# Kernel optimization log

Measured on AMD Instinct MI355X. Metric: run time of the kernel, lower is better.

Reference implementation:

```python
import jax, jax.numpy as jnp
import numpy as np

N = 50000      # nodes
E = 800000     # edges (avg degree 16)
D = 128        # enc_input_dim
H = 4          # enc_num_heads
C = 32         # enc_hidden_dim (per head)
OUT = 64       # linear_output_dim
NEG_SLOPE = 0.2


def setup_inputs() -> dict:
    key = jax.random.key(0)
    ks = jax.random.split(key, 12)
    def glorot(k, shape, fan):
        return (jax.random.normal(k, shape, jnp.float32) / np.sqrt(fan)).astype(jnp.float32)
    x = jax.random.normal(ks[0], (N, D), jnp.float32)
    edge_index = jax.random.randint(ks[1], (2, E), 0, N, dtype=jnp.int64)
    # GAT layer 0: in=D, out=C per head, heads=H, concat -> H*C
    W0 = glorot(ks[2], (D, H * C), D)
    att_src0 = glorot(ks[3], (H, C), C)
    att_dst0 = glorot(ks[4], (H, C), C)
    b0 = jnp.zeros((H * C,), jnp.float32)
    # GAT layer 1: in=H*C, out=D, heads=1
    W1 = glorot(ks[5], (H * C, D), H * C)
    att_src1 = glorot(ks[6], (1, D), D)
    att_dst1 = glorot(ks[7], (1, D), D)
    b1 = jnp.zeros((D,), jnp.float32)
    # projection heads
    Wn = glorot(ks[8], (D, OUT), D)
    bn = jnp.zeros((OUT,), jnp.float32)
    We = glorot(ks[9], (D, OUT), D)
    be = jnp.zeros((OUT,), jnp.float32)
    return dict(x=x, edge_index=edge_index,
                W0=W0, att_src0=att_src0, att_dst0=att_dst0, b0=b0,
                W1=W1, att_src1=att_src1, att_dst1=att_dst1, b1=b1,
                Wn=Wn, bn=bn, We=We, be=be)


def gat_conv(x, src, dst, W, att_s, att_d, b):
    # PyG GATConv: project, per-head attention logits, LeakyReLU,
    # softmax over incoming edges per destination node, scatter-add aggregate.
    n = x.shape[0]
    heads, ch = att_s.shape
    xl = (x @ W).reshape(n, heads, ch)                       # [N,H,C]
    a_s = jnp.einsum('nhc,hc->nh', xl, att_s)                # [N,H]
    a_d = jnp.einsum('nhc,hc->nh', xl, att_d)                # [N,H]
    alpha = jax.nn.leaky_relu(a_s[src] + a_d[dst], NEG_SLOPE)  # [E',H]
    amax = jax.lax.stop_gradient(jax.ops.segment_max(alpha, dst, num_segments=n))
    ex = jnp.exp(alpha - amax[dst])
    denom = jax.ops.segment_sum(ex, dst, num_segments=n)
    w = ex / (denom[dst] + 1e-16)                            # [E',H]
    out = jax.ops.segment_sum(xl[src] * w[:, :, None], dst, num_segments=n)
    return out.reshape(n, heads * ch) + b


def reference(x, edge_index, W0, att_src0, att_dst0, b0,
              W1, att_src1, att_dst1, b1, Wn, bn, We, be):
    n = x.shape[0]
    loop = jnp.arange(n, dtype=edge_index.dtype)             # PyG add_self_loops
    src = jnp.concatenate([edge_index[0], loop])
    dst = jnp.concatenate([edge_index[1], loop])
    h = jax.nn.relu(gat_conv(x, src, dst, W0, att_src0, att_dst0, b0))
    h = jax.nn.relu(gat_conv(h, src, dst, W1, att_src1, att_dst1, b1))
    h_neighbor = h @ Wn + bn
    h_ego = x @ We + be
    return (h_ego, h_neighbor)
```

## Files before the change

kernel.cpp:

```cpp
#include <hip/hip_runtime.h>


#define LEAKY_SLOPE 0.2f
#define BUCKET_CAP 64

typedef __attribute__((ext_vector_type(8))) short s16x8;
typedef __attribute__((ext_vector_type(4))) float f32x4;

static __device__ __forceinline__ unsigned short f2bf(float f)
{
    unsigned x = __float_as_uint(f);
    unsigned r = (x + 0x7fffu + ((x >> 16) & 1u)) >> 16;
    return (unsigned short)r;
}
static __device__ __forceinline__ float bfhi(unsigned u) { return __uint_as_float(u & 0xffff0000u); }
static __device__ __forceinline__ float bflo(unsigned u) { return __uint_as_float(u << 16); }

__global__ __launch_bounds__(256) void init_k(const float* __restrict__ W0,
                                              const float* __restrict__ W1,
                                              const float* __restrict__ Wn,
                                              const float* __restrict__ We,
                                              unsigned short* __restrict__ P0,
                                              unsigned short* __restrict__ P1,
                                              unsigned short* __restrict__ Pn,
                                              unsigned short* __restrict__ Pe,
                                              int4* __restrict__ curs4, int nz4)
{
    int gid = blockIdx.x * 256 + threadIdx.x;
    if (gid < nz4) {
        curs4[gid] = make_int4(0, 0, 0, 0);
        return;
    }
    int idx = gid - nz4;
    if (idx < 49152) {
        const float* S; unsigned short* D; int BN; int local;
        if (idx < 16384)      { S = W0; D = P0; BN = 128; local = idx; }
        else if (idx < 32768) { S = W1; D = P1; BN = 128; local = idx - 16384; }
        else if (idx < 40960) { S = Wn; D = Pn; BN = 64;  local = idx - 32768; }
        else                  { S = We; D = Pe; BN = 64;  local = idx - 40960; }
        int k = local / BN, nn = local % BN;
        D[(((k >> 3) * BN + nn) * 8) + (k & 7)] = f2bf(S[local]);
    }
}

template<int HATT, bool AF32>
static __device__ __forceinline__ void gemm128_body(int tile,
                                                    const void* __restrict__ Ab,
                                                    const unsigned short* __restrict__ Bp,
                                                    unsigned short* __restrict__ Cb,
                                                    const float* __restrict__ ats,
                                                    const float* __restrict__ atd,
                                                    float* __restrict__ a_s,
                                                    float* __restrict__ a_d, int n,
                                                    char* __restrict__ sm)
{
    constexpr int BN = 128;
    constexpr int APITCH = 144;
    constexpr int BPITCH = BN + 2;

    unsigned short* As = (unsigned short*)sm;
    unsigned short* Bs = (unsigned short*)(sm + 64 * APITCH * 2);
    float* smS = (float*)(sm + 64 * APITCH * 2 + 16 * BPITCH * 8 * 2);
    float* smD = smS + 128;

    const int t  = threadIdx.x;
    const int rb = tile * 64;

#pragma unroll
    for (int i = 0; i < 4; ++i) {
        int q = t + i * 256;
        int r = q >> 4;
        int c = (q & 15) * 8;
        int gr = rb + r;
        if (AF32) {
            uint4 o = make_uint4(0u, 0u, 0u, 0u);
            if (gr < n) {
                const float* src = (const float*)Ab + (size_t)gr * 128 + c;
                float4 v0 = *(const float4*)src;
                float4 v1 = *(const float4*)(src + 4);
                o.x = (unsigned)f2bf(v0.x) | ((unsigned)f2bf(v0.y) << 16);
                o.y = (unsigned)f2bf(v0.z) | ((unsigned)f2bf(v0.w) << 16);
                o.z = (unsigned)f2bf(v1.x) | ((unsigned)f2bf(v1.y) << 16);
                o.w = (unsigned)f2bf(v1.z) | ((unsigned)f2bf(v1.w) << 16);
            }
            *(uint4*)(As + r * APITCH + c) = o;
        } else {
            float4 v = make_float4(0.f, 0.f, 0.f, 0.f);
            if (gr < n) v = *(const float4*)((const unsigned short*)Ab + (size_t)gr * 128 + c);
            *(float4*)(As + r * APITCH + c) = v;
        }
    }
#pragma unroll
    for (int i = 0; i < 8; ++i) {
        int ge = t + i * 256;
        int o = ge / BN, nn = ge % BN;
        *(float4*)(Bs + ((size_t)o * BPITCH + nn) * 8) = *(const float4*)(Bp + (size_t)ge * 8);
    }
    __syncthreads();

    const int w = t >> 6, lane = t & 63;
    const int m = lane & 15, quad = lane >> 4;
    const int wc = w & 1, wr = w >> 1;
    const int row0 = wr * 32;
    const int col0 = wc * 64;

    f32x4 acc[2][4];
#pragma unroll
    for (int rt = 0; rt < 2; ++rt)
#pragma unroll
        for (int c = 0; c < 4; ++c) acc[rt][c] = (f32x4){0.f, 0.f, 0.f, 0.f};

    s16x8 a[2][4];
#pragma unroll
    for (int rt = 0; rt < 2; ++rt)
#pragma unroll
        for (int kk = 0; kk < 4; ++kk)
            a[rt][kk] = *(const s16x8*)(As + (row0 + rt * 16 + m) * APITCH + kk * 32 + quad * 8);

#pragma unroll
    for (int kk = 0; kk < 4; ++kk)
#pragma unroll
        for (int c = 0; c < 4; ++c) {
            s16x8 b = *(const s16x8*)(Bs + ((size_t)(kk * 4 + quad) * BPITCH + col0 + c * 16 + m) * 8);
#pragma unroll
            for (int rt = 0; rt < 2; ++rt)
                acc[rt][c] = __builtin_amdgcn_mfma_f32_16x16x32_bf16(a[rt][kk], b, acc[rt][c], 0, 0, 0);
        }

#pragma unroll
    for (int rt = 0; rt < 2; ++rt)
#pragma unroll
        for (int c = 0; c < 4; ++c)
#pragma unroll
            for (int r = 0; r < 4; ++r) {
                int row = rb + row0 + rt * 16 + quad * 4 + r;
                int colg = col0 + c * 16 + m;
                if (row < n) Cb[(size_t)row * 128 + colg] = f2bf(acc[rt][c][r]);
            }

    float atsv[4], atdv[4];
#pragma unroll
    for (int c = 0; c < 4; ++c) {
        atsv[c] = ats[col0 + c * 16 + m];
        atdv[c] = atd[col0 + c * 16 + m];
    }
    if (HATT == 4) {
#pragma unroll
        for (int rt = 0; rt < 2; ++rt)
#pragma unroll
            for (int r = 0; r < 4; ++r)
#pragma unroll
                for (int hb = 0; hb < 2; ++hb) {
                    float ps = acc[rt][2*hb][r] * atsv[2*hb] + acc[rt][2*hb+1][r] * atsv[2*hb+1];
                    float pd = acc[rt][2*hb][r] * atdv[2*hb] + acc[rt][2*hb+1][r] * atdv[2*hb+1];
#pragma unroll
                    for (int off = 1; off < 16; off <<= 1) {
                        ps += __shfl_xor(ps, off);
                        pd += __shfl_xor(pd, off);
                    }
                    int row = rb + row0 + rt * 16 + quad * 4 + r;
                    if (m == 0 && row < n) {
                        a_s[(size_t)row * 4 + 2*wc + hb] = ps;
                        a_d[(size_t)row * 4 + 2*wc + hb] = pd;
                    }
                }
    }
    if (HATT == 1) {
#pragma unroll
        for (int rt = 0; rt < 2; ++rt)
#pragma unroll
            for (int r = 0; r < 4; ++r) {
                float ps = 0.f, pd = 0.f;
#pragma unroll
                for (int c = 0; c < 4; ++c) {
                    ps = fmaf(acc[rt][c][r], atsv[c], ps);
                    pd = fmaf(acc[rt][c][r], atdv[c], pd);
                }
#pragma unroll
                for (int off = 1; off < 16; off <<= 1) {
                    ps += __shfl_xor(ps, off);
                    pd += __shfl_xor(pd, off);
                }
                int lrow = row0 + rt * 16 + quad * 4 + r;
                if (m == 0) { smS[lrow * 2 + wc] = ps; smD[lrow * 2 + wc] = pd; }
            }
        __syncthreads();
        if (t < 64) {
            int row = rb + t;
            if (row < n) {
                a_s[row] = smS[t * 2 + 0] + smS[t * 2 + 1];
                a_d[row] = smD[t * 2 + 0] + smD[t * 2 + 1];
            }
        }
    }
}

template<bool AF32>
static __device__ __forceinline__ void proj64_body(int tile,
                                                   const void* __restrict__ Ab,
                                                   const unsigned short* __restrict__ Bp,
                                                   const float* __restrict__ bias,
                                                   float* __restrict__ Cf, int n,
                                                   char* __restrict__ sm)
{
    constexpr int BN = 64;
    constexpr int APITCH = 144;
    constexpr int BPITCH = BN + 2;

    unsigned short* As = (unsigned short*)sm;
    unsigned short* Bs = (unsigned short*)(sm + 64 * APITCH * 2);

    const int t  = threadIdx.x;
    const int rb = tile * 64;

#pragma unroll
    for (int i = 0; i < 4; ++i) {
        int q = t + i * 256;
        int r = q >> 4;
        int c = (q & 15) * 8;
        int gr = rb + r;
        if (AF32) {
            uint4 o = make_uint4(0u, 0u, 0u, 0u);
            if (gr < n) {
                const float* src = (const float*)Ab + (size_t)gr * 128 + c;
                float4 v0 = *(const float4*)src;
                float4 v1 = *(const float4*)(src + 4);
                o.x = (unsigned)f2bf(v0.x) | ((unsigned)f2bf(v0.y) << 16);
                o.y = (unsigned)f2bf(v0.z) | ((unsigned)f2bf(v0.w) << 16);
                o.z = (unsigned)f2bf(v1.x) | ((unsigned)f2bf(v1.y) << 16);
                o.w = (unsigned)f2bf(v1.z) | ((unsigned)f2bf(v1.w) << 16);
            }
            *(uint4*)(As + r * APITCH + c) = o;
        } else {
            float4 v = make_float4(0.f, 0.f, 0.f, 0.f);
            if (gr < n) v = *(const float4*)((const unsigned short*)Ab + (size_t)gr * 128 + c);
            *(float4*)(As + r * APITCH + c) = v;
        }
    }
#pragma unroll
    for (int i = 0; i < 4; ++i) {
        int ge = t + i * 256;
        int o = ge / BN, nn = ge % BN;
        *(float4*)(Bs + ((size_t)o * BPITCH + nn) * 8) = *(const float4*)(Bp + (size_t)ge * 8);
    }
    __syncthreads();

    const int w = t >> 6, lane = t & 63;
    const int m = lane & 15, quad = lane >> 4;
    const int row0 = w * 16;

    f32x4 acc[4];
#pragma unroll
    for (int c = 0; c < 4; ++c) acc[c] = (f32x4){0.f, 0.f, 0.f, 0.f};

    s16x8 a[4];
#pragma unroll
    for (int kk = 0; kk < 4; ++kk)
        a[kk] = *(const s16x8*)(As + (row0 + m) * APITCH + kk * 32 + quad * 8);

#pragma unroll
    for (int kk = 0; kk < 4; ++kk)
#pragma unroll
        for (int c = 0; c < 4; ++c) {
            s16x8 b = *(const s16x8*)(Bs + ((size_t)(kk * 4 + quad) * BPITCH + c * 16 + m) * 8);
            acc[c] = __builtin_amdgcn_mfma_f32_16x16x32_bf16(a[kk], b, acc[c], 0, 0, 0);
        }

#pragma unroll
    for (int c = 0; c < 4; ++c)
#pragma unroll
        for (int r = 0; r < 4; ++r) {
            int row = rb + row0 + quad * 4 + r;
            int colg = c * 16 + m;
            if (row < n) Cf[(size_t)row * BN + colg] = acc[c][r] + bias[colg];
        }
}

__global__ __launch_bounds__(256) void build_k(const float* __restrict__ x,
                                               const unsigned short* __restrict__ P0,
                                               const unsigned short* __restrict__ Pe,
                                               unsigned short* __restrict__ xlb,
                                               const float* __restrict__ ats,
                                               const float* __restrict__ atd,
                                               float* __restrict__ a_s,
                                               float* __restrict__ a_d,
                                               const float* __restrict__ be,
                                               float* __restrict__ Ce,
                                               const int* __restrict__ ei,
                                               int* __restrict__ curs,
                                               unsigned short* __restrict__ col,
                                               int E, int n,
                                               int scatBlocks, int gemmBlocks)
{
    extern __shared__ char sm[];
    int b = blockIdx.x;
    if (b < scatBlocks) {
        int t8 = (b * 256 + threadIdx.x) * 8;
        if (t8 < E) {
            if ((E & 7) == 0) {
                int4 s0 = *(const int4*)(ei + t8);
                int4 s1 = *(const int4*)(ei + t8 + 4);
                int4 d0 = *(const int4*)(ei + E + t8);
                int4 d1 = *(const int4*)(ei + E + t8 + 4);
                int p0 = atomicAdd(&curs[d0.x << 4], 1);
                int p1 = atomicAdd(&curs[d0.y << 4], 1);
                int p2 = atomicAdd(&curs[d0.z << 4], 1);
                int p3 = atomicAdd(&curs[d0.w << 4], 1);
                int p4 = atomicAdd(&curs[d1.x << 4], 1);
                int p5 = atomicAdd(&curs[d1.y << 4], 1);
                int p6 = atomicAdd(&curs[d1.z << 4], 1);
                int p7 = atomicAdd(&curs[d1.w << 4], 1);
                if (p0 < BUCKET_CAP) col[(d0.x << 6) + p0] = (unsigned short)s0.x;
                if (p1 < BUCKET_CAP) col[(d0.y << 6) + p1] = (unsigned short)s0.y;
                if (p2 < BUCKET_CAP) col[(d0.z << 6) + p2] = (unsigned short)s0.z;
                if (p3 < BUCKET_CAP) col[(d0.w << 6) + p3] = (unsigned short)s0.w;
                if (p4 < BUCKET_CAP) col[(d1.x << 6) + p4] = (unsigned short)s1.x;
                if (p5 < BUCKET_CAP) col[(d1.y << 6) + p5] = (unsigned short)s1.y;
                if (p6 < BUCKET_CAP) col[(d1.z << 6) + p6] = (unsigned short)s1.z;
                if (p7 < BUCKET_CAP) col[(d1.w << 6) + p7] = (unsigned short)s1.w;
            } else {
                int lim = (t8 + 8 < E) ? t8 + 8 : E;
                for (int e = t8; e < lim; ++e) {
                    int s = ei[e], d = ei[E + e];
                    int p = atomicAdd(&curs[d << 4], 1);
                    if (p < BUCKET_CAP) col[(d << 6) + p] = (unsigned short)s;
                }
            }
        }
    } else if (b < scatBlocks + gemmBlocks) {
        gemm128_body<4, true>(b - scatBlocks, x, P0, xlb, ats, atd, a_s, a_d, n, sm);
    } else {
        proj64_body<true>(b - scatBlocks - gemmBlocks, x, Pe, be, Ce, n, sm);
    }
}

__global__ __launch_bounds__(256) void gemm1_k(const unsigned short* __restrict__ Ab,
                                               const unsigned short* __restrict__ Bp,
                                               unsigned short* __restrict__ Cb,
                                               const float* __restrict__ ats,
                                               const float* __restrict__ atd,
                                               float* __restrict__ a_s,
                                               float* __restrict__ a_d, int n)
{
    extern __shared__ char sm[];
    gemm128_body<1, false>(blockIdx.x, Ab, Bp, Cb, ats, atd, a_s, a_d, n, sm);
}

__global__ __launch_bounds__(256) void projN_k(const unsigned short* __restrict__ Ab,
                                               const unsigned short* __restrict__ Bp,
                                               const float* __restrict__ bias,
                                               float* __restrict__ Cf, int n)
{
    extern __shared__ char sm[];
    proj64_body<false>(blockIdx.x, Ab, Bp, bias, Cf, n, sm);
}

template<int H>
__global__ __launch_bounds__(256) void agg_k(const unsigned short* __restrict__ xlb,
                                             const float* __restrict__ a_s,
                                             const float* __restrict__ a_d,
                                             const int* __restrict__ curs,
                                             const unsigned short* __restrict__ col,
                                             const float* __restrict__ bias,
                                             unsigned short* __restrict__ outb, int n)
{
    int node = (blockIdx.x * 256 + threadIdx.x) >> 6;
    int lane = threadIdx.x & 63;
    if (node >= n) return;
    const int sub = lane >> 5, sl = lane & 31;
    const int h = (H == 1) ? 0 : (sl >> 3);
    float ad = a_d[(size_t)node * H + h];
    int m = curs[node << 4];
    if (m > BUCKET_CAP) m = BUCKET_CAP;
    float a0 = 0.f, a1 = 0.f, a2 = 0.f, a3 = 0.f, den = 0.f;
    const unsigned short* xlj = xlb + 4 * sl;

    if (m > 0) {
        int p0 = node << 6;
        int cv = col[p0 + (lane < m ? lane : m - 1)];
        int j = 0;
        for (; j + 16 <= m; j += 16) {
            int jb = j + 8 * sub;
            int s[8]; float as[8]; uint2 uv[8];
#pragma unroll
            for (int q = 0; q < 8; ++q) s[q] = __shfl(cv, jb + q);
#pragma unroll
            for (int q = 0; q < 8; ++q) as[q] = a_s[(size_t)s[q] * H + h];
#pragma unroll
            for (int q = 0; q < 8; ++q) uv[q] = *(const uint2*)(xlj + (size_t)s[q] * 128);
#pragma unroll
            for (int q = 0; q < 8; ++q) {
                float al = as[q] + ad;
                al = (al >= 0.f) ? al : LEAKY_SLOPE * al;
                float w = __expf(al);
                a0 = fmaf(w, bflo(uv[q].x), a0);
                a1 = fmaf(w, bfhi(uv[q].x), a1);
                a2 = fmaf(w, bflo(uv[q].y), a2);
                a3 = fmaf(w, bfhi(uv[q].y), a3);
                den += w;
            }
        }
        int rem = m - j;
        if (rem > 0) {
            int cnt = sub ? (rem > 8 ? rem - 8 : 0) : (rem < 8 ? rem : 8);
            int jb = j + 8 * sub;
            int s[8]; float as[8]; uint2 uv[8];
#pragma unroll
            for (int q = 0; q < 8; ++q) s[q] = __shfl(cv, (q < cnt) ? (jb + q) : j);
#pragma unroll
            for (int q = 0; q < 8; ++q) as[q] = a_s[(size_t)s[q] * H + h];
#pragma unroll
            for (int q = 0; q < 8; ++q) uv[q] = *(const uint2*)(xlj + (size_t)s[q] * 128);
#pragma unroll
            for (int q = 0; q < 8; ++q) {
                float al = as[q] + ad;
                al = (al >= 0.f) ? al : LEAKY_SLOPE * al;
                float w = (q < cnt) ? __expf(al) : 0.f;
                a0 = fmaf(w, bflo(uv[q].x), a0);
                a1 = fmaf(w, bfhi(uv[q].x), a1);
                a2 = fmaf(w, bflo(uv[q].y), a2);
                a3 = fmaf(w, bfhi(uv[q].y), a3);
                den += w;
            }
        }
    }

    a0 += __shfl_xor(a0, 32);
    a1 += __shfl_xor(a1, 32);
    a2 += __shfl_xor(a2, 32);
    a3 += __shfl_xor(a3, 32);
    den += __shfl_xor(den, 32);

    if (sub == 0) {
        float asv = a_s[(size_t)node * H + h];
        float als = asv + ad;
        als = (als >= 0.f) ? als : LEAKY_SLOPE * als;
        float ws = __expf(als);
        uint2 uvs = *(const uint2*)(xlj + (size_t)node * 128);
        a0 = fmaf(ws, bflo(uvs.x), a0);
        a1 = fmaf(ws, bfhi(uvs.x), a1);
        a2 = fmaf(ws, bflo(uvs.y), a2);
        a3 = fmaf(ws, bfhi(uvs.y), a3);
        den += ws;

        float inv = 1.0f / (den + 1e-16f);
        int j = 4 * sl;
        float o0 = fmaxf(fmaf(a0, inv, bias[j]),     0.f);
        float o1 = fmaxf(fmaf(a1, inv, bias[j + 1]), 0.f);
        float o2 = fmaxf(fmaf(a2, inv, bias[j + 2]), 0.f);
        float o3 = fmaxf(fmaf(a3, inv, bias[j + 3]), 0.f);
        uint2 pk;
        pk.x = (unsigned)f2bf(o0) | ((unsigned)f2bf(o1) << 16);
        pk.y = (unsigned)f2bf(o2) | ((unsigned)f2bf(o3) << 16);
        *(uint2*)(outb + (size_t)node * 128 + j) = pk;
    }
}

extern "C" void kernel_launch(void* const* d_in, const int* in_sizes, int n_in,
                              void* d_out, int out_size, void* d_ws, size_t ws_size,
                              hipStream_t stream)
{
    const float* x   = (const float*)d_in[0];
    const int*   ei  = (const int*)d_in[1];
    const float* W0  = (const float*)d_in[2];
    const float* as0 = (const float*)d_in[3];
    const float* ad0 = (const float*)d_in[4];
    const float* b0  = (const float*)d_in[5];
    const float* W1  = (const float*)d_in[6];
    const float* as1 = (const float*)d_in[7];
    const float* ad1 = (const float*)d_in[8];
    const float* b1  = (const float*)d_in[9];
    const float* Wn  = (const float*)d_in[10];
    const float* bn  = (const float*)d_in[11];
    const float* We  = (const float*)d_in[12];
    const float* be  = (const float*)d_in[13];

    const int n  = in_sizes[0] / 128;
    const int E  = in_sizes[1] / 2;
    float* out = (float*)d_out;

    char* w = (char*)d_ws;
    auto carve = [&](size_t bytes) -> void* {
        void* p = (void*)w;
        w += (bytes + 255) & ~(size_t)255;
        return p;
    };
    unsigned short* xlb = (unsigned short*)carve((size_t)n * 128 * 2);
    unsigned short* hb  = (unsigned short*)carve((size_t)n * 128 * 2);
    float* a_s  = (float*)carve((size_t)n * 4 * 4);
    float* a_d  = (float*)carve((size_t)n * 4 * 4);
    int*   curs = (int*)carve((size_t)n * 16 * 4);
    unsigned short* colv = (unsigned short*)carve((size_t)n * BUCKET_CAP * 2);
    unsigned short* P0 = (unsigned short*)carve(16384 * 2);
    unsigned short* P1 = (unsigned short*)carve(16384 * 2);
    unsigned short* Pn = (unsigned short*)carve(8192 * 2);
    unsigned short* Pe = (unsigned short*)carve(8192 * 2);

    const int gN64  = (n + 63) / 64;
    const int gWv   = (n + 3) / 4;
    const int gScat = ((E + 7) / 8 + 255) / 256;
    const int initWork = n * 4 + 49152;

    constexpr int GEMM_SM  = 64 * 144 * 2 + 16 * 130 * 8 * 2;
    constexpr int GEMM1_SM = GEMM_SM + 1024;
    constexpr int PROJ_SM  = 64 * 144 * 2 + 16 * 66 * 8 * 2;

    init_k<<<(initWork + 255) / 256, 256, 0, stream>>>(W0, W1, Wn, We,
                                                       P0, P1, Pn, Pe,
                                                       (int4*)curs, n * 4);

    build_k<<<gScat + 2 * gN64, 256, GEMM_SM, stream>>>(x, P0, Pe, xlb, as0, ad0,
                                                        a_s, a_d, be, out,
                                                        ei, curs, colv, E, n,
                                                        gScat, gN64);

    agg_k<4><<<gWv, 256, 0, stream>>>(xlb, a_s, a_d, curs, colv, b0, hb, n);

    gemm1_k<<<gN64, 256, GEMM1_SM, stream>>>(hb, P1, xlb, as1, ad1, a_s, a_d, n);

    agg_k<1><<<gWv, 256, 0, stream>>>(xlb, a_s, a_d, curs, colv, b1, hb, n);

    projN_k<<<gN64, 256, PROJ_SM, stream>>>(hb, Pn, bn, out + (size_t)n * 64, n);
}
```

Baseline: 238.6 us.

## Fuse GAT aggregation with following dense projection into per-16-node MFMA kernels

Replaces the separate aggregate, layer-1 GEMM, aggregate and final projection kernels with two fused kernels. Each block aggregates 16 nodes using 16 lanes per node with 16-byte gathers, stages the resulting hidden rows in shared memory, then multiplies them by W1 or Wn with MFMA and writes the next layer's features plus attention logits, or the final output. This removes two launches and the global round trip of the intermediate hidden tensors. In exchange, every 16-node block reloads the full weight matrix into shared memory, and each wave's MFMA work is small, so the per-block setup cost is amortised over few rows.

```diff
diff --git a/kernel.cpp b/kernel.cpp
--- a/kernel.cpp
+++ b/kernel.cpp
@@ -60,8 +60,6 @@
 
     unsigned short* As = (unsigned short*)sm;
     unsigned short* Bs = (unsigned short*)(sm + 64 * APITCH * 2);
-    float* smS = (float*)(sm + 64 * APITCH * 2 + 16 * BPITCH * 8 * 2);
-    float* smD = smS + 128;
 
     const int t  = threadIdx.x;
     const int rb = tile * 64;
@@ -164,34 +162,6 @@
                         a_d[(size_t)row * 4 + 2*wc + hb] = pd;
                     }
                 }
-    }
-    if (HATT == 1) {
-#pragma unroll
-        for (int rt = 0; rt < 2; ++rt)
-#pragma unroll
-            for (int r = 0; r < 4; ++r) {
-                float ps = 0.f, pd = 0.f;
-#pragma unroll
-                for (int c = 0; c < 4; ++c) {
-                    ps = fmaf(acc[rt][c][r], atsv[c], ps);
-                    pd = fmaf(acc[rt][c][r], atdv[c], pd);
-                }
-#pragma unroll
-                for (int off = 1; off < 16; off <<= 1) {
-                    ps += __shfl_xor(ps, off);
-                    pd += __shfl_xor(pd, off);
-                }
-                int lrow = row0 + rt * 16 + quad * 4 + r;
-                if (m == 0) { smS[lrow * 2 + wc] = ps; smD[lrow * 2 + wc] = pd; }
-            }
-        __syncthreads();
-        if (t < 64) {
-            int row = rb + t;
-            if (row < n) {
-                a_s[row] = smS[t * 2 + 0] + smS[t * 2 + 1];
-                a_d[row] = smD[t * 2 + 0] + smD[t * 2 + 1];
-            }
-        }
     }
 }
 
@@ -334,125 +304,190 @@
     }
 }
 
-__global__ __launch_bounds__(256) void gemm1_k(const unsigned short* __restrict__ Ab,
-                                               const unsigned short* __restrict__ Bp,
-                                               unsigned short* __restrict__ Cb,
-                                               const float* __restrict__ ats,
-                                               const float* __restrict__ atd,
-                                               float* __restrict__ a_s,
-                                               float* __restrict__ a_d, int n)
-{
+template<int LAYER>
+__global__ __launch_bounds__(256) void agg_mv_k(const unsigned short* __restrict__ xin,
+                                                const float* __restrict__ asi,
+                                                const float* __restrict__ adi,
+                                                const int* __restrict__ curs,
+                                                const unsigned short* __restrict__ col,
+                                                const float* __restrict__ bpre,
+                                                const unsigned short* __restrict__ Wp,
+                                                const float* __restrict__ ats,
+                                                const float* __restrict__ atd,
+                                                unsigned short* __restrict__ xlo,
+                                                float* __restrict__ aso,
+                                                float* __restrict__ ado,
+                                                const float* __restrict__ bpost,
+                                                float* __restrict__ outf,
+                                                int n)
+{
+    constexpr int H      = (LAYER == 0) ? 4 : 1;
+    constexpr int BN     = (LAYER == 0) ? 128 : 64;
+    constexpr int BPITCH = BN + 2;
+
     extern __shared__ char sm[];
-    gemm128_body<1, false>(blockIdx.x, Ab, Bp, Cb, ats, atd, a_s, a_d, n, sm);
-}
-
-__global__ __launch_bounds__(256) void projN_k(const unsigned short* __restrict__ Ab,
-                                               const unsigned short* __restrict__ Bp,
-                                               const float* __restrict__ bias,
-                                               float* __restrict__ Cf, int n)
-{
-    extern __shared__ char sm[];
-    proj64_body<false>(blockIdx.x, Ab, Bp, bias, Cf, n, sm);
-}
-
-template<int H>
-__global__ __launch_bounds__(256) void agg_k(const unsigned short* __restrict__ xlb,
-                                             const float* __restrict__ a_s,
-                                             const float* __restrict__ a_d,
-                                             const int* __restrict__ curs,
-                                             const unsigned short* __restrict__ col,
-                                             const float* __restrict__ bias,
-                                             unsigned short* __restrict__ outb, int n)
-{
-    int node = (blockIdx.x * 256 + threadIdx.x) >> 6;
-    int lane = threadIdx.x & 63;
-    if (node >= n) return;
-    const int sub = lane >> 5, sl = lane & 31;
-    const int h = (H == 1) ? 0 : (sl >> 3);
-    float ad = a_d[(size_t)node * H + h];
-    int m = curs[node << 4];
-    if (m > BUCKET_CAP) m = BUCKET_CAP;
-    float a0 = 0.f, a1 = 0.f, a2 = 0.f, a3 = 0.f, den = 0.f;
-    const unsigned short* xlj = xlb + 4 * sl;
-
-    if (m > 0) {
-        int p0 = node << 6;
-        int cv = col[p0 + (lane < m ? lane : m - 1)];
-        int j = 0;
-        for (; j + 16 <= m; j += 16) {
-            int jb = j + 8 * sub;
-            int s[8]; float as[8]; uint2 uv[8];
-#pragma unroll
-            for (int q = 0; q < 8; ++q) s[q] = __shfl(cv, jb + q);
-#pragma unroll
-            for (int q = 0; q < 8; ++q) as[q] = a_s[(size_t)s[q] * H + h];
-#pragma unroll
-            for (int q = 0; q < 8; ++q) uv[q] = *(const uint2*)(xlj + (size_t)s[q] * 128);
+    unsigned short* Bs   = (unsigned short*)sm;
+    unsigned short* hrow = (unsigned short*)(sm + 16 * BPITCH * 8 * 2);
+    float* smS = (float*)(sm + 16 * BPITCH * 8 * 2 + 16 * 128 * 2);
+    float* smD = smS + 64;
+
+    const int t = threadIdx.x;
+
+#pragma unroll
+    for (int i = 0; i < BN / 16; ++i) {
+        int ge = t + i * 256;
+        int o = ge / BN, nn2 = ge % BN;
+        *(float4*)(Bs + ((size_t)o * BPITCH + nn2) * 8) = *(const float4*)(Wp + (size_t)ge * 8);
+    }
+
+    const int nd   = t >> 4;
+    const int L16  = t & 15;
+    const int lane = t & 63;
+    const int gb   = lane & 48;
+    const int node = blockIdx.x * 16 + nd;
+    const int h    = (LAYER == 0) ? (L16 >> 2) : 0;
+
+    if (node < n) {
+        float c0=0.f,c1=0.f,c2=0.f,c3=0.f,c4=0.f,c5=0.f,c6=0.f,c7=0.f,den=0.f;
+        float ad = adi[(size_t)node * H + h];
+        int m = curs[node << 4];
+        if (m > BUCKET_CAP) m = BUCKET_CAP;
+        const unsigned short* xbase = xin + L16 * 8;
+        const int p0 = node << 6;
+
+        int cvu = 0;
+        for (int j = 0; j < m; j += 8) {
+            if ((j & 15) == 0) cvu = col[p0 + j + L16];
+            int cnt = m - j; if (cnt > 8) cnt = 8;
+            int sq[8]; float as8[8]; uint4 uv[8];
 #pragma unroll
             for (int q = 0; q < 8; ++q) {
-                float al = as[q] + ad;
+                int idx = (q < cnt) ? (j + q) : j;
+                sq[q] = __shfl(cvu, gb + (idx & 15));
+            }
+#pragma unroll
+            for (int q = 0; q < 8; ++q) as8[q] = asi[(size_t)sq[q] * H + h];
+#pragma unroll
+            for (int q = 0; q < 8; ++q) uv[q] = *(const uint4*)(xbase + (size_t)sq[q] * 128);
+#pragma unroll
+            for (int q = 0; q < 8; ++q) {
+                float al = as8[q] + ad;
                 al = (al >= 0.f) ? al : LEAKY_SLOPE * al;
-                float w = __expf(al);
-                a0 = fmaf(w, bflo(uv[q].x), a0);
-                a1 = fmaf(w, bfhi(uv[q].x), a1);
-                a2 = fmaf(w, bflo(uv[q].y), a2);
-                a3 = fmaf(w, bfhi(uv[q].y), a3);
-                den += w;
-            }
-        }
-        int rem = m - j;
-        if (rem > 0) {
-            int cnt = sub ? (rem > 8 ? rem - 8 : 0) : (rem < 8 ? rem : 8);
-            int jb = j + 8 * sub;
-            int s[8]; float as[8]; uint2 uv[8];
-#pragma unroll
-            for (int q = 0; q < 8; ++q) s[q] = __shfl(cv, (q < cnt) ? (jb + q) : j);
-#pragma unroll
-            for (int q = 0; q < 8; ++q) as[q] = a_s[(size_t)s[q] * H + h];
-#pragma unroll
-            for (int q = 0; q < 8; ++q) uv[q] = *(const uint2*)(xlj + (size_t)s[q] * 128);
-#pragma unroll
-            for (int q = 0; q < 8; ++q) {
-                float al = as[q] + ad;
-                al = (al >= 0.f) ? al : LEAKY_SLOPE * al;
-                float w = (q < cnt) ? __expf(al) : 0.f;
-                a0 = fmaf(w, bflo(uv[q].x), a0);
-                a1 = fmaf(w, bfhi(uv[q].x), a1);
-                a2 = fmaf(w, bflo(uv[q].y), a2);
-                a3 = fmaf(w, bfhi(uv[q].y), a3);
-                den += w;
-            }
-        }
-    }
-
-    a0 += __shfl_xor(a0, 32);
-    a1 += __shfl_xor(a1, 32);
-    a2 += __shfl_xor(a2, 32);
-    a3 += __shfl_xor(a3, 32);
-    den += __shfl_xor(den, 32);
-
-    if (sub == 0) {
-        float asv = a_s[(size_t)node * H + h];
-        float als = asv + ad;
-        als = (als >= 0.f) ? als : LEAKY_SLOPE * als;
-        float ws = __expf(als);
-        uint2 uvs = *(const uint2*)(xlj + (size_t)node * 128);
-        a0 = fmaf(ws, bflo(uvs.x), a0);
-        a1 = fmaf(ws, bfhi(uvs.x), a1);
-        a2 = fmaf(ws, bflo(uvs.y), a2);
-        a3 = fmaf(ws, bfhi(uvs.y), a3);
-        den += ws;
-
+                float wq = (q < cnt) ? __expf(al) : 0.f;
+                c0 = fmaf(wq, bflo(uv[q].x), c0);
+                c1 = fmaf(wq, bfhi(uv[q].x), c1);
+                c2 = fmaf(wq, bflo(uv[q].y), c2);
+                c3 = fmaf(wq, bfhi(uv[q].y), c3);
+                c4 = fmaf(wq, bflo(uv[q].z), c4);
+                c5 = fmaf(wq, bfhi(uv[q].z), c5);
+                c6 = fmaf(wq, bflo(uv[q].w), c6);
+                c7 = fmaf(wq, bfhi(uv[q].w), c7);
+                den += wq;
+            }
+        }
+        {
+            float sv = asi[(size_t)node * H + h];
+            float al = sv + ad;
+            al = (al >= 0.f) ? al : LEAKY_SLOPE * al;
+            float ws = __expf(al);
+            uint4 uvs = *(const uint4*)(xbase + (size_t)node * 128);
+            c0 = fmaf(ws, bflo(uvs.x), c0);
+            c1 = fmaf(ws, bfhi(uvs.x), c1);
+            c2 = fmaf(ws, bflo(uvs.y), c2);
+            c3 = fmaf(ws, bfhi(uvs.y), c3);
+            c4 = fmaf(ws, bflo(uvs.z), c4);
+            c5 = fmaf(ws, bfhi(uvs.z), c5);
+            c6 = fmaf(ws, bflo(uvs.w), c6);
+            c7 = fmaf(ws, bfhi(uvs.w), c7);
+            den += ws;
+        }
         float inv = 1.0f / (den + 1e-16f);
-        int j = 4 * sl;
-        float o0 = fmaxf(fmaf(a0, inv, bias[j]),     0.f);
-        float o1 = fmaxf(fmaf(a1, inv, bias[j + 1]), 0.f);
-        float o2 = fmaxf(fmaf(a2, inv, bias[j + 2]), 0.f);
-        float o3 = fmaxf(fmaf(a3, inv, bias[j + 3]), 0.f);
-        uint2 pk;
-        pk.x = (unsigned)f2bf(o0) | ((unsigned)f2bf(o1) << 16);
-        pk.y = (unsigned)f2bf(o2) | ((unsigned)f2bf(o3) << 16);
-        *(uint2*)(outb + (size_t)node * 128 + j) = pk;
+        const float* bp = bpre + L16 * 8;
+        float h0v = fmaxf(fmaf(c0, inv, bp[0]), 0.f);
+        float h1v = fmaxf(fmaf(c1, inv, bp[1]), 0.f);
+        float h2v = fmaxf(fmaf(c2, inv, bp[2]), 0.f);
+        float h3v = fmaxf(fmaf(c3, inv, bp[3]), 0.f);
+        float h4v = fmaxf(fmaf(c4, inv, bp[4]), 0.f);
+        float h5v = fmaxf(fmaf(c5, inv, bp[5]), 0.f);
+        float h6v = fmaxf(fmaf(c6, inv, bp[6]), 0.f);
+        float h7v = fmaxf(fmaf(c7, inv, bp[7]), 0.f);
+        uint4 hv;
+        hv.x = (unsigned)f2bf(h0v) | ((unsigned)f2bf(h1v) << 16);
+        hv.y = (unsigned)f2bf(h2v) | ((unsigned)f2bf(h3v) << 16);
+        hv.z = (unsigned)f2bf(h4v) | ((unsigned)f2bf(h5v) << 16);
+        hv.w = (unsigned)f2bf(h6v) | ((unsigned)f2bf(h7v) << 16);
+        *(uint4*)(hrow + nd * 128 + L16 * 8) = hv;
+    } else {
+        *(uint4*)(hrow + nd * 128 + L16 * 8) = make_uint4(0u, 0u, 0u, 0u);
+    }
+
+    __syncthreads();
+
+    const int w    = t >> 6;
+    const int m16  = lane & 15;
+    const int quad = lane >> 4;
+
+    s16x8 afr[4];
+#pragma unroll
+    for (int kk = 0; kk < 4; ++kk)
+        afr[kk] = *(const s16x8*)(hrow + m16 * 128 + kk * 32 + quad * 8);
+
+    if (LAYER == 0) {
+        f32x4 acc[2];
+        acc[0] = (f32x4){0.f, 0.f, 0.f, 0.f};
+        acc[1] = (f32x4){0.f, 0.f, 0.f, 0.f};
+#pragma unroll
+        for (int kk = 0; kk < 4; ++kk)
+#pragma unroll
+            for (int ct = 0; ct < 2; ++ct) {
+                int colg = (w * 2 + ct) * 16 + m16;
+                s16x8 b = *(const s16x8*)(Bs + ((size_t)(kk * 4 + quad) * BPITCH + colg) * 8);
+                acc[ct] = __builtin_amdgcn_mfma_f32_16x16x32_bf16(afr[kk], b, acc[ct], 0, 0, 0);
+            }
+#pragma unroll
+        for (int r = 0; r < 4; ++r) {
+            int gnode = blockIdx.x * 16 + quad * 4 + r;
+            float ps = 0.f, pd = 0.f;
+#pragma unroll
+            for (int ct = 0; ct < 2; ++ct) {
+                int colg = (w * 2 + ct) * 16 + m16;
+                float v = acc[ct][r];
+                if (gnode < n) xlo[(size_t)gnode * 128 + colg] = f2bf(v);
+                ps = fmaf(v, ats[colg], ps);
+                pd = fmaf(v, atd[colg], pd);
+            }
+#pragma unroll
+            for (int off = 1; off < 16; off <<= 1) {
+                ps += __shfl_xor(ps, off);
+                pd += __shfl_xor(pd, off);
+            }
+            if (m16 == 0) {
+                smS[(quad * 4 + r) * 4 + w] = ps;
+                smD[(quad * 4 + r) * 4 + w] = pd;
+            }
+        }
+        __syncthreads();
+        if (t < 16) {
+            int gnode = blockIdx.x * 16 + t;
+            if (gnode < n) {
+                aso[gnode] = smS[t * 4] + smS[t * 4 + 1] + smS[t * 4 + 2] + smS[t * 4 + 3];
+                ado[gnode] = smD[t * 4] + smD[t * 4 + 1] + smD[t * 4 + 2] + smD[t * 4 + 3];
+            }
+        }
+    } else {
+        f32x4 acc = (f32x4){0.f, 0.f, 0.f, 0.f};
+        int colg = w * 16 + m16;
+#pragma unroll
+        for (int kk = 0; kk < 4; ++kk) {
+            s16x8 b = *(const s16x8*)(Bs + ((size_t)(kk * 4 + quad) * BPITCH + colg) * 8);
+            acc = __builtin_amdgcn_mfma_f32_16x16x32_bf16(afr[kk], b, acc, 0, 0, 0);
+        }
+        float bv = bpost[colg];
+#pragma unroll
+        for (int r = 0; r < 4; ++r) {
+            int gnode = blockIdx.x * 16 + quad * 4 + r;
+            if (gnode < n) outf[(size_t)gnode * 64 + colg] = acc[r] + bv;
+        }
     }
 }
 
@@ -487,8 +522,10 @@
     };
     unsigned short* xlb = (unsigned short*)carve((size_t)n * 128 * 2);
     unsigned short* hb  = (unsigned short*)carve((size_t)n * 128 * 2);
-    float* a_s  = (float*)carve((size_t)n * 4 * 4);
-    float* a_d  = (float*)carve((size_t)n * 4 * 4);
+    float* a_s0 = (float*)carve((size_t)n * 4 * 4);
+    float* a_d0 = (float*)carve((size_t)n * 4 * 4);
+    float* a_s1 = (float*)carve((size_t)n * 4);
+    float* a_d1 = (float*)carve((size_t)n * 4);
     int*   curs = (int*)carve((size_t)n * 16 * 4);
     unsigned short* colv = (unsigned short*)carve((size_t)n * BUCKET_CAP * 2);
     unsigned short* P0 = (unsigned short*)carve(16384 * 2);
@@ -497,28 +534,30 @@
     unsigned short* Pe = (unsigned short*)carve(8192 * 2);
 
     const int gN64  = (n + 63) / 64;
-    const int gWv   = (n + 3) / 4;
+    const int gB16  = (n + 15) / 16;
     const int gScat = ((E + 7) / 8 + 255) / 256;
     const int initWork = n * 4 + 49152;
 
-    constexpr int GEMM_SM  = 64 * 144 * 2 + 16 * 130 * 8 * 2;
-    constexpr int GEMM1_SM = GEMM_SM + 1024;
-    constexpr int PROJ_SM  = 64 * 144 * 2 + 16 * 66 * 8 * 2;
+    constexpr int GEMM_SM = 64 * 144 * 2 + 16 * 130 * 8 * 2;
+    constexpr int AGG0_SM = 16 * 130 * 8 * 2 + 16 * 128 * 2 + 512;
+    constexpr int AGG1_SM = 16 * 66 * 8 * 2 + 16 * 128 * 2 + 512;
 
     init_k<<<(initWork + 255) / 256, 256, 0, stream>>>(W0, W1, Wn, We,
                                                        P0, P1, Pn, Pe,
                                                        (int4*)curs, n * 4);
 
     build_k<<<gScat + 2 * gN64, 256, GEMM_SM, stream>>>(x, P0, Pe, xlb, as0, ad0,
-                                                        a_s, a_d, be, out,
+                                                        a_s0, a_d0, be, out,
                                                         ei, curs, colv, E, n,
                                                         gScat, gN64);
 
-    agg_k<4><<<gWv, 256, 0, stream>>>(xlb, a_s, a_d, curs, colv, b0, hb, n);
-
-    gemm1_k<<<gN64, 256, GEMM1_SM, stream>>>(hb, P1, xlb, as1, ad1, a_s, a_d, n);
-
-    agg_k<1><<<gWv, 256, 0, stream>>>(xlb, a_s, a_d, curs, colv, b1, hb, n);
-
-    projN_k<<<gN64, 256, PROJ_SM, stream>>>(hb, Pn, bn, out + (size_t)n * 64, n);
-}
+    agg_mv_k<0><<<gB16, 256, AGG0_SM, stream>>>(xlb, a_s0, a_d0, curs, colv, b0,
+                                                P1, as1, ad1,
+                                                hb, a_s1, a_d1,
+                                                nullptr, nullptr, n);
+
+    agg_mv_k<1><<<gB16, 256, AGG1_SM, stream>>>(hb, a_s1, a_d1, curs, colv, b1,
+                                                Pn, nullptr, nullptr,
+                                                nullptr, nullptr, nullptr,
+                                                bn, out + (size_t)n * 64, n);
+}
```

Result: faster. 220.7 us (-7.5%).
